# Kernel tuning notes

Measured on AMD Instinct MI355X. Metric: run time of the kernel, lower is better.

## Reference

```python
import jax, jax.numpy as jnp
import numpy as np

B, S, D, H = 4, 1024, 1024, 16
DK = D // H
MASK_WEIGHT_0 = 1.0   # weight for key-type 0 (from (weight, mask_mat) tuple)
MASK_WEIGHT_1 = 0.5   # weight for key-type 1
NEG_INF = -1.0e9


def setup_inputs() -> dict:
    key = jax.random.key(0)
    ks = jax.random.split(key, 10)
    wscale = 0.02
    return {
        "query": jax.random.normal(ks[0], (B, S, D), jnp.float32),
        "key_x": jax.random.normal(ks[1], (B, S, D), jnp.float32),
        "value": jax.random.normal(ks[2], (B, S, D), jnp.float32),
        "mask0": jax.random.randint(ks[3], (B, S, S), 0, 2, jnp.int32),
        "mask1": jax.random.randint(ks[4], (B, S, S), 0, 2, jnp.int32),
        "Wq":  wscale * jax.random.normal(ks[5], (D, D), jnp.float32),
        "Wk0": wscale * jax.random.normal(ks[6], (D, D), jnp.float32),
        "Wk1": wscale * jax.random.normal(ks[7], (D, D), jnp.float32),
        "Wv":  wscale * jax.random.normal(ks[8], (D, D), jnp.float32),
        "Wo":  wscale * jax.random.normal(ks[9], (D, D), jnp.float32),
    }


def _heads(x, W):
    # torch nn.Linear: x @ W.T ; then view(B,S,H,DK).transpose(1,2)
    return (x @ W.T).reshape(B, S, H, DK).transpose(0, 2, 1, 3)  # [B,H,S,DK]


def reference(query, key_x, value, mask0, mask1, Wq, Wk0, Wk1, Wv, Wo):
    q = _heads(query, Wq)          # [B,H,S,DK]
    k0 = _heads(key_x, Wk0)
    k1 = _heads(key_x, Wk1)
    v = _heads(value, Wv)
    scale = 1.0 / jnp.sqrt(jnp.float32(DK))

    def masked_score(k, mask, weight):
        s = jnp.einsum('bhqd,bhkd->bhqk', q, k) * scale       # [B,H,S,S]
        keep = (mask != 0)[:, None, :, :]                     # broadcast over heads
        # (score * weight*keep).masked_fill(mask==0, -1e9)
        return jnp.where(keep, s * weight, NEG_INF)

    scores = masked_score(k0, mask0, MASK_WEIGHT_0) + masked_score(k1, mask1, MASK_WEIGHT_1)
    p_attn = jax.nn.sigmoid(scores)                           # activation='sigmoid'
    x = jnp.einsum('bhqk,bhkd->bhqd', p_attn, v)              # [B,H,S,DK]
    x = x.transpose(0, 2, 1, 3).reshape(B, S, D)
    return x @ Wo.T                                            # output_linear (dropout p=0)
```

## Files before the change

kernel.cpp:

```cpp
#include <hip/hip_runtime.h>

#define B_  4
#define S_  1024
#define D_  1024
#define H_  16
#define DK_ 64

typedef __attribute__((ext_vector_type(8)))  short bf16x8;
typedef __attribute__((ext_vector_type(4)))  short bf16x4;
typedef __attribute__((ext_vector_type(4)))  float f32x4;
typedef __attribute__((ext_vector_type(16))) float f32x16;

static __device__ __forceinline__ unsigned short f2bf(float f) {
  union { float f; unsigned u; } v; v.f = f;
  unsigned r = v.u + 0x7FFFu + ((v.u >> 16) & 1u);
  return (unsigned short)(r >> 16);
}

static __device__ __forceinline__ unsigned cvtpk(float lo, float hi) {
  unsigned r;
  asm("v_cvt_pk_bf16_f32 %0, %1, %2" : "=v"(r) : "v"(lo), "v"(hi));
  return r;
}
static __device__ __forceinline__ void plswap(unsigned &a, unsigned &b) {
  asm volatile("v_permlane32_swap_b32 %0, %1" : "+v"(a), "+v"(b));
}

typedef __attribute__((address_space(1))) const void gc_t;
typedef __attribute__((address_space(3))) void lds_t;
static __device__ __forceinline__ void gload_lds16(const void* g, void* l) {
  __builtin_amdgcn_global_load_lds((gc_t*)g, (lds_t*)l, 16, 0, 0);
}

#define TM_ (1u << 22)
#define WM_ (1u << 20)

#define CEXP_ (-0.18033688011112042f)

__global__ __launch_bounds__(256)
void prep(const float* __restrict__ q, const float* __restrict__ k,
          const float* __restrict__ v,
          const float* __restrict__ w0, const float* __restrict__ w1,
          const float* __restrict__ w2, const float* __restrict__ w3,
          const float* __restrict__ w4, unsigned short* __restrict__ out,
          const int* __restrict__ m0, const int* __restrict__ m1,
          unsigned long long* __restrict__ pk)
{
  if (blockIdx.x < 4096) {
    const size_t u = ((size_t)blockIdx.x * 256 + threadIdx.x) * 16;
    unsigned short t[16];
    unsigned short* dst;
    if (u < (size_t)3 * TM_) {
      const int seg = (int)(u >> 22);
      const size_t off = u & (TM_ - 1);
      const float* src = seg == 0 ? q : (seg == 1 ? k : v);
      dst = out + (size_t)seg * TM_ + off;
      float4 f[4];
#pragma unroll
      for (int i = 0; i < 4; ++i) f[i] = *(const float4*)(src + off + 4*i);
#pragma unroll
      for (int i = 0; i < 4; ++i) {
        t[4*i]   = f2bf(f[i].x); t[4*i+1] = f2bf(f[i].y);
        t[4*i+2] = f2bf(f[i].z); t[4*i+3] = f2bf(f[i].w);
      }
    } else {
      const size_t uu = u - (size_t)3 * TM_;
      const int seg = (int)(uu >> 20);
      const size_t off = uu & (WM_ - 1);
      dst = out + (size_t)3 * TM_ + (size_t)seg * WM_ + off;
      if (seg == 1) {
        float4 a[4], b[4];
#pragma unroll
        for (int i = 0; i < 4; ++i) a[i] = *(const float4*)(w1 + off + 4*i);
#pragma unroll
        for (int i = 0; i < 4; ++i) b[i] = *(const float4*)(w2 + off + 4*i);
#pragma unroll
        for (int i = 0; i < 4; ++i) {
          t[4*i]   = f2bf(a[i].x + 0.5f*b[i].x);
          t[4*i+1] = f2bf(a[i].y + 0.5f*b[i].y);
          t[4*i+2] = f2bf(a[i].z + 0.5f*b[i].z);
          t[4*i+3] = f2bf(a[i].w + 0.5f*b[i].w);
        }
      } else {
        const float sc = (seg == 0) ? CEXP_ : 1.0f;
        const float* src = (seg == 0) ? w0 : (seg == 2 ? w3 : w4);
        float4 f[4];
#pragma unroll
        for (int i = 0; i < 4; ++i) f[i] = *(const float4*)(src + off + 4*i);
#pragma unroll
        for (int i = 0; i < 4; ++i) {
          t[4*i]   = f2bf(sc*f[i].x); t[4*i+1] = f2bf(sc*f[i].y);
          t[4*i+2] = f2bf(sc*f[i].z); t[4*i+3] = f2bf(sc*f[i].w);
        }
      }
    }
    *(bf16x8*)dst       = *(bf16x8*)&t[0];
    *(bf16x8*)(dst + 8) = *(bf16x8*)&t[8];
  } else {
    const int row = (blockIdx.x - 4096) * 4 + (threadIdx.x >> 6);
    const int lw  = threadIdx.x & 63;
    const int4* m0p = (const int4*)(m0 + (size_t)row * 1024);
    const int4* m1p = (const int4*)(m1 + (size_t)row * 1024);
    int4 a[4], b[4];
#pragma unroll
    for (int c = 0; c < 4; ++c) { a[c] = m0p[c*64 + lw]; b[c] = m1p[c*64 + lw]; }
    unsigned long long* pkrow = pk + (size_t)row * 16;
#pragma unroll
    for (int c = 0; c < 4; ++c) {
      const unsigned long long b0 = __ballot((a[c].x != 0) & (b[c].x != 0));
      const unsigned long long b1 = __ballot((a[c].y != 0) & (b[c].y != 0));
      const unsigned long long b2 = __ballot((a[c].z != 0) & (b[c].z != 0));
      const unsigned long long b3 = __ballot((a[c].w != 0) & (b[c].w != 0));
      unsigned long long wv[4];
#pragma unroll
      for (int w = 0; w < 4; ++w) {
        wv[w] =  ((b0 >> (16*w)) & 0xFFFFull)
              | (((b1 >> (16*w)) & 0xFFFFull) << 16)
              | (((b2 >> (16*w)) & 0xFFFFull) << 32)
              | (((b3 >> (16*w)) & 0xFFFFull) << 48);
      }
      const unsigned long long sel =
          (lw == 0) ? wv[0] : (lw == 1) ? wv[1] : (lw == 2) ? wv[2] : wv[3];
      if (lw < 4) pkrow[c*4 + lw] = sel;
    }
  }
}

__global__ __launch_bounds__(256, 4)
void proj_gemm(const unsigned short* __restrict__ qbf,
               const unsigned short* __restrict__ kbf,
               const unsigned short* __restrict__ vbf,
               const unsigned short* __restrict__ wbf,
               unsigned short* __restrict__ Qb, unsigned short* __restrict__ Kh,
               unsigned short* __restrict__ Vth)
{
  __shared__ unsigned short As[128][64];
  __shared__ unsigned short Ws[128][64];

  const int tid = threadIdx.x, bid = blockIdx.x;
  const int xcd = bid & 7, c = bid >> 3;
  const int L = xcd * 96 + c;
  const int which = L >> 8;
  const int rem = L & 255;
  const int nt = rem >> 5, mt = rem & 31;
  const int m0 = mt * 128, n0 = nt * 128;
  const int w = tid >> 6, l = tid & 63;
  const int lr = l & 15, lg = l >> 4;
  const int wr = w >> 1, wc = w & 1;

  const unsigned short* A = (which == 0) ? qbf : (which == 1) ? kbf : vbf;
  const unsigned short* W = wbf + (size_t)which * WM_;

  const f32x4 fzero = {0.f, 0.f, 0.f, 0.f};
  f32x4 acc[4][4];
#pragma unroll
  for (int m = 0; m < 4; m++)
#pragma unroll
    for (int n = 0; n < 4; n++) acc[m][n] = fzero;

  const int srow8 = l >> 3;
  const int sg    = ((l & 7) ^ srow8) * 8;
  const int rc0 = ((lg)     ^ (lr & 7)) * 8;
  const int rc1 = ((4 + lg) ^ (lr & 7)) * 8;

  const unsigned short* aBase = A + (size_t)(m0 + w*32 + srow8) * 1024 + sg;
  const unsigned short* wBase = W + (size_t)(n0 + w*32 + srow8) * 1024 + sg;

  for (int kk = 0; kk < 1024; kk += 64) {
#pragma unroll
    for (int cc = 0; cc < 4; ++cc)
      gload_lds16(aBase + (size_t)cc * 8 * 1024 + kk, &As[w*32 + cc*8][0]);
#pragma unroll
    for (int cc = 0; cc < 4; ++cc)
      gload_lds16(wBase + (size_t)cc * 8 * 1024 + kk, &Ws[w*32 + cc*8][0]);
    __syncthreads();

#pragma unroll
    for (int ks = 0; ks < 2; ++ks) {
      const int rc = ks ? rc1 : rc0;
      bf16x8 af[4], bfr[4];
#pragma unroll
      for (int m = 0; m < 4; m++) af[m]  = *(const bf16x8*)&As[wr*64 + m*16 + lr][rc];
#pragma unroll
      for (int n = 0; n < 4; n++) bfr[n] = *(const bf16x8*)&Ws[wc*64 + n*16 + lr][rc];
#pragma unroll
      for (int m = 0; m < 4; m++)
#pragma unroll
        for (int n = 0; n < 4; n++)
          acc[m][n] = __builtin_amdgcn_mfma_f32_16x16x32_bf16(af[m], bfr[n], acc[m][n], 0, 0, 0);
    }
    __syncthreads();
  }

  if (which == 2) {
#pragma unroll
    for (int m = 0; m < 4; m++) {
      const int row = m0 + wr*64 + m*16 + lg*4;
      const int b = row >> 10, s = row & 1023;
#pragma unroll
      for (int n = 0; n < 4; n++) {
        const int col = n0 + wc*64 + n*16 + lr;
        const int h = col >> 6, dk = col & 63;
        unsigned short tv[4] = {f2bf(acc[m][n][0]), f2bf(acc[m][n][1]),
                                f2bf(acc[m][n][2]), f2bf(acc[m][n][3])};
        const size_t a = ((size_t)((b*H_ + h)*DK_ + dk)) * S_
                       + (size_t)(s & ~63) + ((((s >> 3) & 7) ^ (dk & 7)) << 3) + (s & 7);
        *(bf16x4*)(Vth + a) = *(bf16x4*)tv;
      }
    }
  } else if (which == 0) {
#pragma unroll
    for (int m = 0; m < 4; m++) {
      const int row = m0 + wr*64 + m*16 + lg*4;
#pragma unroll
      for (int n = 0; n < 4; n++) {
        const int col = n0 + wc*64 + n*16 + lr;
#pragma unroll
        for (int r = 0; r < 4; r++)
          Qb[(size_t)(row + r) * 1024 + col] = f2bf(acc[m][n][r]);
      }
    }
  } else {
#pragma unroll
    for (int m = 0; m < 4; m++) {
      const int row = m0 + wr*64 + m*16 + lg*4;
#pragma unroll
      for (int n = 0; n < 4; n++) {
        const int col = n0 + wc*64 + n*16 + lr;
        const int h = col >> 6, dk = col & 63;
#pragma unroll
        for (int r = 0; r < 4; r++) {
          const int rr = row + r;
          const int b = rr >> 10, s = rr & 1023;
          const size_t a = ((size_t)((b*H_ + h)*S_ + s)) * 64
                         + (((dk >> 3) ^ (s & 7)) << 3) + (dk & 7);
          Kh[a] = f2bf(acc[m][n][r]);
        }
      }
    }
  }
}

__global__ __launch_bounds__(256, 4)
void out_gemm(const unsigned short* __restrict__ A,
              const unsigned short* __restrict__ W, float* __restrict__ C)
{
  __shared__ unsigned short As[128][64];
  __shared__ unsigned short Ws2[64][64];

  const int tid = threadIdx.x, bid = blockIdx.x;
  const int xcd = bid & 7, idx = bid >> 3;
  const int mt = (xcd << 2) | (idx & 3);
  const int nt = idx >> 2;
  const int m0 = mt * 128, n0 = nt * 64;
  const int w = tid >> 6, l = tid & 63;
  const int lr = l & 15, lg = l >> 4;
  const int wr = w >> 1, wc = w & 1;

  const f32x4 fzero = {0.f, 0.f, 0.f, 0.f};
  f32x4 acc[4][2];
#pragma unroll
  for (int m = 0; m < 4; m++)
#pragma unroll
    for (int n = 0; n < 2; n++) acc[m][n] = fzero;

  const int srow8 = l >> 3;
  const int sg    = ((l & 7) ^ srow8) * 8;
  const int rc0 = ((lg)     ^ (lr & 7)) * 8;
  const int rc1 = ((4 + lg) ^ (lr & 7)) * 8;

  const unsigned short* aBase = A + (size_t)(m0 + w*32 + srow8) * 1024 + sg;
  const unsigned short* wBase = W + (size_t)(n0 + w*16 + srow8) * 1024 + sg;

  for (int kk = 0; kk < 1024; kk += 64) {
#pragma unroll
    for (int cc = 0; cc < 4; ++cc)
      gload_lds16(aBase + (size_t)cc * 8 * 1024 + kk, &As[w*32 + cc*8][0]);
#pragma unroll
    for (int cc = 0; cc < 2; ++cc)
      gload_lds16(wBase + (size_t)cc * 8 * 1024 + kk, &Ws2[w*16 + cc*8][0]);
    __syncthreads();

#pragma unroll
    for (int ks = 0; ks < 2; ++ks) {
      const int rc = ks ? rc1 : rc0;
      bf16x8 af[4], bfr[2];
#pragma unroll
      for (int m = 0; m < 4; m++) af[m]  = *(const bf16x8*)&As[wr*64 + m*16 + lr][rc];
#pragma unroll
      for (int n = 0; n < 2; n++) bfr[n] = *(const bf16x8*)&Ws2[wc*32 + n*16 + lr][rc];
#pragma unroll
      for (int m = 0; m < 4; m++)
#pragma unroll
        for (int n = 0; n < 2; n++)
          acc[m][n] = __builtin_amdgcn_mfma_f32_16x16x32_bf16(af[m], bfr[n], acc[m][n], 0, 0, 0);
    }
    __syncthreads();
  }

#pragma unroll
  for (int m = 0; m < 4; m++) {
    const int row = m0 + wr*64 + m*16 + lg*4;
#pragma unroll
    for (int n = 0; n < 2; n++) {
      const int col = n0 + wc*32 + n*16 + lr;
#pragma unroll
      for (int r = 0; r < 4; r++)
        C[(size_t)(row + r) * 1024 + col] = acc[m][n][r];
    }
  }
}

__global__ __launch_bounds__(512)
void attn_kernel(const unsigned short* __restrict__ Q,
                 const unsigned short* __restrict__ Kh,
                 const unsigned short* __restrict__ Vth,
                 const unsigned long long* __restrict__ mpk,
                 unsigned short* __restrict__ X)
{
  __shared__ unsigned short Ks[2][2][4096];
  __shared__ unsigned short Vs[2][2][4096];

  const int tid  = threadIdx.x;
  const int bid0 = blockIdx.x;
  const int bid = ((bid0 & 7) << 6) | (bid0 >> 3);
  const int qt = bid & 7, h = (bid >> 3) & 15, b = bid >> 7;
  const int q0 = qt * 128;
  const int w8 = tid >> 6, lw = tid & 63;
  const int grp = w8 >> 2, qw = w8 & 3;
  const int l31 = lw & 31, hh = lw >> 5, l7 = lw & 7;
  const int bh = b * H_ + h;

  bf16x8 qf[4];
  {
    const unsigned short* qp = Q + ((size_t)(b*S_ + q0 + qw*32 + l31)) * D_ + h*DK_ + hh*8;
#pragma unroll
    for (int ds = 0; ds < 4; ++ds) qf[ds] = *(const bf16x8*)(qp + ds*16);
  }
  const size_t mbase = ((size_t)(b*S_ + q0 + qw*32 + l31)) * 16 + grp*8;

  f32x16 acc0, acc1;
#pragma unroll
  for (int r = 0; r < 16; ++r) { acc0[r] = 0.f; acc1[r] = 0.f; }

  const unsigned short* gp[4];
  unsigned short* lb[4];
  int stp[4];
#pragma unroll
  for (int c = 0; c < 4; ++c) {
    const int e = qw*4 + c;
    const int bu = e >> 3, s = e & 7;
    lb[c] = (bu == 0 ? &Ks[grp][0][0] : &Vs[grp][0][0]) + s*512;
    if (bu == 0) {
      gp[c]  = Kh + (size_t)bh * 65536 + grp*32768 + s*512 + lw*8;
      stp[c] = 4096;
    } else {
      gp[c]  = Vth + ((size_t)(bh*DK_ + s*8 + (lw >> 3))) * S_ + grp*512 + (lw & 7) * 8;
      stp[c] = 64;
    }
  }

#define STAGE(nxt)                                                     \
  {                                                                    \
    _Pragma("unroll")                                                  \
    for (int c = 0; c < 4; ++c) {                                      \
      gload_lds16(gp[c], lb[c] + (nxt)*4096);                          \
      gp[c] += stp[c];                                                 \
    }                                                                  \
  }

  STAGE(0);
  __syncthreads();
  unsigned long long mw = mpk[mbase];
  int cur = 0;

  for (int t = 0; t < 8; ++t) {
    unsigned long long mw_n = 0;
    if (t < 7) { STAGE(cur ^ 1); mw_n = mpk[mbase + t + 1]; }

#pragma unroll
    for (int sub = 0; sub < 2; ++sub) {
      const int rbase = (sub*32 + l31) * 64;
      f32x16 sv;
#pragma unroll
      for (int r = 0; r < 16; ++r) sv[r] = 0.f;
      __builtin_amdgcn_s_setprio(1);
#pragma unroll
      for (int ds = 0; ds < 4; ++ds) {
        const int g = (((ds*2 + hh) ^ l7)) * 8;
        const bf16x8 kf = *(const bf16x8*)&Ks[grp][cur][rbase + g];
        sv = __builtin_amdgcn_mfma_f32_32x32x16_bf16(kf, qf[ds], sv, 0, 0, 0);
      }
      __builtin_amdgcn_s_setprio(0);

      const unsigned long long ams = mw >> (8*sub + hh);
      float p[16];
#pragma unroll
      for (int r = 0; r < 16; ++r) {
        const int cbit = 16*(r & 3) + 2*(r >> 2);
        const float e  = __builtin_amdgcn_exp2f(sv[r]);
        const float pr = __builtin_amdgcn_rcpf(1.0f + e);
        p[r] = ((ams >> cbit) & 1ull) ? pr : 0.f;
      }

      bf16x8 pa[2];
#pragma unroll
      for (int ks = 0; ks < 2; ++ks) {
        const int a0 = ks*8;
        unsigned u0 = cvtpk(p[a0+0], p[a0+1]);
        unsigned u1 = cvtpk(p[a0+2], p[a0+3]);
        unsigned u2 = cvtpk(p[a0+4], p[a0+5]);
        unsigned u3 = cvtpk(p[a0+6], p[a0+7]);
        plswap(u0, u2);
        plswap(u1, u3);
        union { unsigned u[4]; bf16x8 v; } pu;
        pu.u[0] = u0; pu.u[1] = u1; pu.u[2] = u2; pu.u[3] = u3;
        pa[ks] = pu.v;
      }

      __builtin_amdgcn_s_setprio(1);
#pragma unroll
      for (int ks = 0; ks < 2; ++ks) {
        const int g = ((sub*4 + ks*2 + hh) ^ l7) * 8;
        const bf16x8 vb0 = *(const bf16x8*)&Vs[grp][cur][(l31)      * 64 + g];
        const bf16x8 vb1 = *(const bf16x8*)&Vs[grp][cur][(32 + l31) * 64 + g];
        acc0 = __builtin_amdgcn_mfma_f32_32x32x16_bf16(pa[ks], vb0, acc0, 0, 0, 0);
        acc1 = __builtin_amdgcn_mfma_f32_32x32x16_bf16(pa[ks], vb1, acc1, 0, 0, 0);
      }
      __builtin_amdgcn_s_setprio(0);
    }

    if (t < 7) {
      __syncthreads();
      mw = mw_n;
      cur ^= 1;
    }
  }
#undef STAGE

  __syncthreads();
  float2* cmb = (float2*)&Ks[0][0][0];
  if (grp == 1) {
#pragma unroll
    for (int i = 0; i < 8; ++i)
      cmb[(qw*16 + i)*64 + lw] = make_float2(acc0[2*i], acc0[2*i+1]);
#pragma unroll
    for (int i = 0; i < 8; ++i)
      cmb[(qw*16 + 8 + i)*64 + lw] = make_float2(acc1[2*i], acc1[2*i+1]);
  }
  __syncthreads();
  if (grp == 0) {
#pragma unroll
    for (int i = 0; i < 8; ++i) {
      float2 v = cmb[(qw*16 + i)*64 + lw];
      acc0[2*i] += v.x; acc0[2*i+1] += v.y;
    }
#pragma unroll
    for (int i = 0; i < 8; ++i) {
      float2 v = cmb[(qw*16 + 8 + i)*64 + lw];
      acc1[2*i] += v.x; acc1[2*i+1] += v.y;
    }
#pragma unroll
    for (int r = 0; r < 16; ++r) {
      const int qrow = q0 + qw*32 + (r & 3) + 8*(r >> 2) + 4*hh;
      unsigned short* xp = X + ((size_t)(b*S_ + qrow)) * D_ + h*DK_ + l31;
      xp[0]  = f2bf(acc0[r]);
      xp[32] = f2bf(acc1[r]);
    }
  }
}

extern "C" void kernel_launch(void* const* d_in, const int* in_sizes, int n_in,
                              void* d_out, int out_size, void* d_ws, size_t ws_size,
                              hipStream_t stream)
{
  const float* query = (const float*)d_in[0];
  const float* key_x = (const float*)d_in[1];
  const float* value = (const float*)d_in[2];
  const int*   mask0 = (const int*)d_in[3];
  const int*   mask1 = (const int*)d_in[4];
  const float* Wq    = (const float*)d_in[5];
  const float* Wk0   = (const float*)d_in[6];
  const float* Wk1   = (const float*)d_in[7];
  const float* Wv    = (const float*)d_in[8];
  const float* Wo    = (const float*)d_in[9];

  unsigned short* ws = (unsigned short*)d_ws;
  unsigned short* qbf = ws;
  unsigned short* kbf = ws + (size_t)TM_;
  unsigned short* vbf = ws + (size_t)2 * TM_;
  unsigned short* wbf = ws + (size_t)3 * TM_;
  unsigned short* Qb  = ws + (size_t)3 * TM_ + 4 * WM_;
  unsigned short* Kh  = Qb  + (size_t)TM_;
  unsigned short* Vth = Kh  + (size_t)TM_;
  unsigned long long* mpk = (unsigned long long*)(Vth + (size_t)TM_);
  unsigned short* Xb = qbf;

  prep<<<dim3(4096 + 1024), dim3(256), 0, stream>>>(
      query, key_x, value, Wq, Wk0, Wk1, Wv, Wo, ws, mask0, mask1, mpk);

  proj_gemm<<<dim3(768), dim3(256), 0, stream>>>(qbf, kbf, vbf, wbf,
                                                 Qb, Kh, Vth);

  attn_kernel<<<dim3(B_ * H_ * (S_ / 128)), dim3(512), 0, stream>>>(
      Qb, Kh, Vth, mpk, Xb);

  out_gemm<<<dim3(512), dim3(256), 0, stream>>>(Xb, wbf + (size_t)3 * WM_,
                                                (float*)d_out);
}
```

Measured before the change: 102.4 us.

## Fuse fp32-to-bf16 activation conversion into projection GEMM and move mask packing

The projection GEMM now reads the fp32 query/key/value activations directly, converts them to bf16 in registers with v_cvt_pk_bf16_f32, and writes them into swizzled LDS. This removes the separate prep pass that wrote bf16 copies of the activations to global memory and read them back. Mask packing moves into extra blocks of the projection kernel, which shrinks the prep kernel to weight conversion only. The trade-off is that the A-tile load now goes through registers instead of direct global-to-LDS loads, which raises register pressure and reads twice as many bytes per tile.

```diff
diff --git a/kernel.cpp b/kernel.cpp
--- a/kernel.cpp
+++ b/kernel.cpp
@@ -38,106 +38,78 @@
 #define CEXP_ (-0.18033688011112042f)
 
 __global__ __launch_bounds__(256)
-void prep(const float* __restrict__ q, const float* __restrict__ k,
-          const float* __restrict__ v,
-          const float* __restrict__ w0, const float* __restrict__ w1,
+void prep(const float* __restrict__ w0, const float* __restrict__ w1,
           const float* __restrict__ w2, const float* __restrict__ w3,
-          const float* __restrict__ w4, unsigned short* __restrict__ out,
-          const int* __restrict__ m0, const int* __restrict__ m1,
-          unsigned long long* __restrict__ pk)
+          const float* __restrict__ w4, unsigned short* __restrict__ wbf)
 {
-  if (blockIdx.x < 4096) {
-    const size_t u = ((size_t)blockIdx.x * 256 + threadIdx.x) * 16;
-    unsigned short t[16];
-    unsigned short* dst;
-    if (u < (size_t)3 * TM_) {
-      const int seg = (int)(u >> 22);
-      const size_t off = u & (TM_ - 1);
-      const float* src = seg == 0 ? q : (seg == 1 ? k : v);
-      dst = out + (size_t)seg * TM_ + off;
-      float4 f[4];
-#pragma unroll
-      for (int i = 0; i < 4; ++i) f[i] = *(const float4*)(src + off + 4*i);
-#pragma unroll
-      for (int i = 0; i < 4; ++i) {
-        t[4*i]   = f2bf(f[i].x); t[4*i+1] = f2bf(f[i].y);
-        t[4*i+2] = f2bf(f[i].z); t[4*i+3] = f2bf(f[i].w);
-      }
-    } else {
-      const size_t uu = u - (size_t)3 * TM_;
-      const int seg = (int)(uu >> 20);
-      const size_t off = uu & (WM_ - 1);
-      dst = out + (size_t)3 * TM_ + (size_t)seg * WM_ + off;
-      if (seg == 1) {
-        float4 a[4], b[4];
-#pragma unroll
-        for (int i = 0; i < 4; ++i) a[i] = *(const float4*)(w1 + off + 4*i);
-#pragma unroll
-        for (int i = 0; i < 4; ++i) b[i] = *(const float4*)(w2 + off + 4*i);
-#pragma unroll
-        for (int i = 0; i < 4; ++i) {
-          t[4*i]   = f2bf(a[i].x + 0.5f*b[i].x);
-          t[4*i+1] = f2bf(a[i].y + 0.5f*b[i].y);
-          t[4*i+2] = f2bf(a[i].z + 0.5f*b[i].z);
-          t[4*i+3] = f2bf(a[i].w + 0.5f*b[i].w);
-        }
-      } else {
-        const float sc = (seg == 0) ? CEXP_ : 1.0f;
-        const float* src = (seg == 0) ? w0 : (seg == 2 ? w3 : w4);
-        float4 f[4];
-#pragma unroll
-        for (int i = 0; i < 4; ++i) f[i] = *(const float4*)(src + off + 4*i);
-#pragma unroll
-        for (int i = 0; i < 4; ++i) {
-          t[4*i]   = f2bf(sc*f[i].x); t[4*i+1] = f2bf(sc*f[i].y);
-          t[4*i+2] = f2bf(sc*f[i].z); t[4*i+3] = f2bf(sc*f[i].w);
-        }
-      }
-    }
-    *(bf16x8*)dst       = *(bf16x8*)&t[0];
-    *(bf16x8*)(dst + 8) = *(bf16x8*)&t[8];
+  const size_t u = ((size_t)blockIdx.x * 256 + threadIdx.x) * 16;
+  const int seg = (int)(u >> 20);
+  const size_t off = u & (WM_ - 1);
+  unsigned short t[16];
+  unsigned short* dst = wbf + (size_t)seg * WM_ + off;
+  if (seg == 1) {
+    float4 a[4], b[4];
+#pragma unroll
+    for (int i = 0; i < 4; ++i) a[i] = *(const float4*)(w1 + off + 4*i);
+#pragma unroll
+    for (int i = 0; i < 4; ++i) b[i] = *(const float4*)(w2 + off + 4*i);
+#pragma unroll
+    for (int i = 0; i < 4; ++i) {
+      t[4*i]   = f2bf(a[i].x + 0.5f*b[i].x);
+      t[4*i+1] = f2bf(a[i].y + 0.5f*b[i].y);
+      t[4*i+2] = f2bf(a[i].z + 0.5f*b[i].z);
+      t[4*i+3] = f2bf(a[i].w + 0.5f*b[i].w);
+    }
   } else {
-    const int row = (blockIdx.x - 4096) * 4 + (threadIdx.x >> 6);
-    const int lw  = threadIdx.x & 63;
-    const int4* m0p = (const int4*)(m0 + (size_t)row * 1024);
-    const int4* m1p = (const int4*)(m1 + (size_t)row * 1024);
-    int4 a[4], b[4];
-#pragma unroll
-    for (int c = 0; c < 4; ++c) { a[c] = m0p[c*64 + lw]; b[c] = m1p[c*64 + lw]; }
-    unsigned long long* pkrow = pk + (size_t)row * 16;
-#pragma unroll
-    for (int c = 0; c < 4; ++c) {
-      const unsigned long long b0 = __ballot((a[c].x != 0) & (b[c].x != 0));
-      const unsigned long long b1 = __ballot((a[c].y != 0) & (b[c].y != 0));
-      const unsigned long long b2 = __ballot((a[c].z != 0) & (b[c].z != 0));
-      const unsigned long long b3 = __ballot((a[c].w != 0) & (b[c].w != 0));
-      unsigned long long wv[4];
-#pragma unroll
-      for (int w = 0; w < 4; ++w) {
-        wv[w] =  ((b0 >> (16*w)) & 0xFFFFull)
-              | (((b1 >> (16*w)) & 0xFFFFull) << 16)
-              | (((b2 >> (16*w)) & 0xFFFFull) << 32)
-              | (((b3 >> (16*w)) & 0xFFFFull) << 48);
-      }
-      const unsigned long long sel =
-          (lw == 0) ? wv[0] : (lw == 1) ? wv[1] : (lw == 2) ? wv[2] : wv[3];
-      if (lw < 4) pkrow[c*4 + lw] = sel;
-    }
-  }
+    const float sc = (seg == 0) ? CEXP_ : 1.0f;
+    const float* src = (seg == 0) ? w0 : (seg == 2 ? w3 : w4);
+    float4 f[4];
+#pragma unroll
+    for (int i = 0; i < 4; ++i) f[i] = *(const float4*)(src + off + 4*i);
+#pragma unroll
+    for (int i = 0; i < 4; ++i) {
+      t[4*i]   = f2bf(sc*f[i].x); t[4*i+1] = f2bf(sc*f[i].y);
+      t[4*i+2] = f2bf(sc*f[i].z); t[4*i+3] = f2bf(sc*f[i].w);
+    }
+  }
+  *(bf16x8*)dst       = *(bf16x8*)&t[0];
+  *(bf16x8*)(dst + 8) = *(bf16x8*)&t[8];
 }
 
 __global__ __launch_bounds__(256, 4)
-void proj_gemm(const unsigned short* __restrict__ qbf,
-               const unsigned short* __restrict__ kbf,
-               const unsigned short* __restrict__ vbf,
+void proj_gemm(const float* __restrict__ qx, const float* __restrict__ kx,
+               const float* __restrict__ vx,
                const unsigned short* __restrict__ wbf,
                unsigned short* __restrict__ Qb, unsigned short* __restrict__ Kh,
-               unsigned short* __restrict__ Vth)
+               unsigned short* __restrict__ Vth,
+               const int* __restrict__ ma, const int* __restrict__ mb,
+               unsigned long long* __restrict__ pk)
 {
   __shared__ unsigned short As[128][64];
   __shared__ unsigned short Ws[128][64];
 
   const int tid = threadIdx.x, bid = blockIdx.x;
+
+  if (bid >= 768) {
+    const int row = bid - 768;
+    const int w4  = tid >> 6, lw = tid & 63;
+    const int4 a  = *(const int4*)(ma + (size_t)row*1024 + w4*256 + lw*4);
+    const int4 b  = *(const int4*)(mb + (size_t)row*1024 + w4*256 + lw*4);
+    const unsigned long long b0 = __ballot((a.x != 0) & (b.x != 0));
+    const unsigned long long b1 = __ballot((a.y != 0) & (b.y != 0));
+    const unsigned long long b2 = __ballot((a.z != 0) & (b.z != 0));
+    const unsigned long long b3 = __ballot((a.w != 0) & (b.w != 0));
+    if (lw < 4) {
+      const unsigned long long wv =
+            ((b0 >> (16*lw)) & 0xFFFFull)
+         | (((b1 >> (16*lw)) & 0xFFFFull) << 16)
+         | (((b2 >> (16*lw)) & 0xFFFFull) << 32)
+         | (((b3 >> (16*lw)) & 0xFFFFull) << 48);
+      pk[(size_t)row*16 + w4*4 + lw] = wv;
+    }
+    return;
+  }
+
   const int xcd = bid & 7, c = bid >> 3;
   const int L = xcd * 96 + c;
   const int which = L >> 8;
@@ -148,7 +120,7 @@
   const int lr = l & 15, lg = l >> 4;
   const int wr = w >> 1, wc = w & 1;
 
-  const unsigned short* A = (which == 0) ? qbf : (which == 1) ? kbf : vbf;
+  const float* Af = (which == 0) ? qx : (which == 1) ? kx : vx;
   const unsigned short* W = wbf + (size_t)which * WM_;
 
   const f32x4 fzero = {0.f, 0.f, 0.f, 0.f};
@@ -158,21 +130,38 @@
 #pragma unroll
     for (int n = 0; n < 4; n++) acc[m][n] = fzero;
 
+  const int r0  = tid >> 3;
+  const int cg  = tid & 7;
+  const int aswz = (cg ^ (r0 & 7)) * 8;
+  const float* aSrc = Af + (size_t)(m0 + r0) * 1024 + cg * 8;
+
   const int srow8 = l >> 3;
   const int sg    = ((l & 7) ^ srow8) * 8;
+  const unsigned short* wBase = W + (size_t)(n0 + w*32 + srow8) * 1024 + sg;
+
   const int rc0 = ((lg)     ^ (lr & 7)) * 8;
   const int rc1 = ((4 + lg) ^ (lr & 7)) * 8;
 
-  const unsigned short* aBase = A + (size_t)(m0 + w*32 + srow8) * 1024 + sg;
-  const unsigned short* wBase = W + (size_t)(n0 + w*32 + srow8) * 1024 + sg;
-
   for (int kk = 0; kk < 1024; kk += 64) {
-#pragma unroll
-    for (int cc = 0; cc < 4; ++cc)
-      gload_lds16(aBase + (size_t)cc * 8 * 1024 + kk, &As[w*32 + cc*8][0]);
+    float4 fa[4][2];
+#pragma unroll
+    for (int p = 0; p < 4; ++p) {
+      const float* s = aSrc + (size_t)(p*32) * 1024 + kk;
+      fa[p][0] = *(const float4*)s;
+      fa[p][1] = *(const float4*)(s + 4);
+    }
 #pragma unroll
     for (int cc = 0; cc < 4; ++cc)
       gload_lds16(wBase + (size_t)cc * 8 * 1024 + kk, &Ws[w*32 + cc*8][0]);
+#pragma unroll
+    for (int p = 0; p < 4; ++p) {
+      union { unsigned u[4]; bf16x8 v; } pu;
+      pu.u[0] = cvtpk(fa[p][0].x, fa[p][0].y);
+      pu.u[1] = cvtpk(fa[p][0].z, fa[p][0].w);
+      pu.u[2] = cvtpk(fa[p][1].x, fa[p][1].y);
+      pu.u[3] = cvtpk(fa[p][1].z, fa[p][1].w);
+      *(bf16x8*)&As[p*32 + r0][aswz] = pu.v;
+    }
     __syncthreads();
 
 #pragma unroll
@@ -486,21 +475,17 @@
   const float* Wo    = (const float*)d_in[9];
 
   unsigned short* ws = (unsigned short*)d_ws;
-  unsigned short* qbf = ws;
-  unsigned short* kbf = ws + (size_t)TM_;
-  unsigned short* vbf = ws + (size_t)2 * TM_;
+  unsigned short* Xb  = ws;
   unsigned short* wbf = ws + (size_t)3 * TM_;
   unsigned short* Qb  = ws + (size_t)3 * TM_ + 4 * WM_;
   unsigned short* Kh  = Qb  + (size_t)TM_;
   unsigned short* Vth = Kh  + (size_t)TM_;
   unsigned long long* mpk = (unsigned long long*)(Vth + (size_t)TM_);
-  unsigned short* Xb = qbf;
-
-  prep<<<dim3(4096 + 1024), dim3(256), 0, stream>>>(
-      query, key_x, value, Wq, Wk0, Wk1, Wv, Wo, ws, mask0, mask1, mpk);
-
-  proj_gemm<<<dim3(768), dim3(256), 0, stream>>>(qbf, kbf, vbf, wbf,
-                                                 Qb, Kh, Vth);
+
+  prep<<<dim3(1024), dim3(256), 0, stream>>>(Wq, Wk0, Wk1, Wv, Wo, wbf);
+
+  proj_gemm<<<dim3(768 + 4096), dim3(256), 0, stream>>>(
+      query, key_x, value, wbf, Qb, Kh, Vth, mask0, mask1, mpk);
 
   attn_kernel<<<dim3(B_ * H_ * (S_ / 128)), dim3(512), 0, stream>>>(
       Qb, Kh, Vth, mpk, Xb);
```

Measured after the change: 111.3 us. 8.8% more time.
